# Kernel optimization log

Measured on AMD Instinct MI355X. Metric: run time of the kernel, lower is better.

## Reference

```python
import jax, jax.numpy as jnp
import numpy as np

V, O, E, D = 256, 128, 1024, 128
EPS = 1e-5


def setup_inputs() -> dict:
    key = jax.random.key(0)
    ks = jax.random.split(key, 8)
    inp = {}
    inp["obj_vecs"] = jax.random.normal(ks[0], (V, O, D), jnp.float32)
    inp["edges"] = jax.random.randint(ks[1], (V, E, 3), 0, O, dtype=jnp.int64)

    def lin(k, out_d, in_d):  # kaiming-ish init
        return jax.random.normal(k, (out_d, in_d), jnp.float32) * np.float32(np.sqrt(2.0 / in_d))

    i = 2
    for u in range(2):
        inp[f"u{u}_g1"] = jnp.ones((2 * D,), jnp.float32)
        inp[f"u{u}_b1"] = jnp.zeros((2 * D,), jnp.float32)
        inp[f"u{u}_W1"] = lin(ks[i], D, 2 * D); i += 1
        inp[f"u{u}_lb1"] = jnp.zeros((D,), jnp.float32)
        inp[f"u{u}_g2"] = jnp.ones((D,), jnp.float32)
        inp[f"u{u}_b2"] = jnp.zeros((D,), jnp.float32)
        inp[f"u{u}_W2"] = lin(ks[i], D, D); i += 1
        inp[f"u{u}_lb2"] = jnp.zeros((D,), jnp.float32)
    return inp


def _bn_relu(x, g, b):
    # training-mode BatchNorm1d (biased var) -> ReLU, pre-activation
    m = jnp.mean(x, axis=0)
    v = jnp.mean(jnp.square(x - m), axis=0)
    return jax.nn.relu((x - m) * jax.lax.rsqrt(v + EPS) * g + b)


def _gconv(x, s_flat, o_flat, p):
    g1, b1, W1, lb1, g2, b2, W2, lb2 = p
    xf = x.reshape(V * O, -1)
    # gather src/dst node features per edge -> (V*E, 2D)
    node = jnp.concatenate([xf[s_flat], xf[o_flat]], axis=-1)
    edge = _bn_relu(node, g1, b1) @ W1.T + lb1  # (V*E, Dedge)
    # scatter_add pooling onto source nodes, then average by in-count
    pooled = jax.ops.segment_sum(edge, s_flat, num_segments=V * O)
    cnt = jax.ops.segment_sum(jnp.ones((V * E,), edge.dtype), s_flat, num_segments=V * O)
    pooled = pooled / jnp.clip(cnt, 1.0)[:, None]
    out = _bn_relu(pooled, g2, b2) @ W2.T + lb2
    return out.reshape(V, O, -1)


def reference(obj_vecs, edges,
              u0_g1, u0_b1, u0_W1, u0_lb1, u0_g2, u0_b2, u0_W2, u0_lb2,
              u1_g1, u1_b1, u1_W1, u1_lb1, u1_g2, u1_b2, u1_W2, u1_lb2):
    off = (jnp.arange(V, dtype=edges.dtype) * O)[:, None]
    s_flat = (off + edges[:, :, 0]).reshape(-1)
    o_flat = (off + edges[:, :, 2]).reshape(-1)
    x = _gconv(obj_vecs, s_flat, o_flat,
               (u0_g1, u0_b1, u0_W1, u0_lb1, u0_g2, u0_b2, u0_W2, u0_lb2))
    x = _gconv(x, s_flat, o_flat,
               (u1_g1, u1_b1, u1_W1, u1_lb1, u1_g2, u1_b2, u1_W2, u1_lb2))
    return x + obj_vecs  # residual (input_dim == output_dim)
```

## Files before the change

kernel.cpp:

```cpp
#include <hip/hip_runtime.h>

namespace {
constexpr int kV = 256, kO = 128, kE = 1024, kD = 128;
constexpr int kN = kV * kO;
constexpr int kVE = kV * kE;
constexpr float kEps = 1e-5f;
}

typedef __attribute__((ext_vector_type(8))) short bf16x8;
typedef __attribute__((ext_vector_type(8))) unsigned short u16x8;
typedef __attribute__((ext_vector_type(4))) float f32x4;

__device__ __forceinline__ unsigned short f2bf(float x) {
  unsigned u = __float_as_uint(x);
  return (unsigned short)((u + 0x7FFFu + ((u >> 16) & 1u)) >> 16);
}
__device__ __forceinline__ float bf2f(unsigned short h) {
  return __uint_as_float((unsigned)h << 16);
}

__global__ __launch_bounds__(256) void k_adj(
    const unsigned int* __restrict__ ew, const float* __restrict__ X,
    int* __restrict__ cnt_s, int* __restrict__ cnt_o,
    unsigned short* __restrict__ Au16, float* __restrict__ p1) {
  __shared__ int cnt[kO * kO];
  __shared__ int degS[kO], degO[kO];
  __shared__ int anyodd;
  int v = blockIdx.x, t = threadIdx.x;
  if (t == 0) anyodd = 0;
  for (int i = t; i < kO * kO; i += 256) cnt[i] = 0;
  __syncthreads();
  int base = v * 3072, loc = 0;
  for (int i = t; i < 3072; i += 256) {
    int g = base + i;
    if ((g & 1) && ew[g] != 0u) loc = 1;
  }
  if (loc) atomicOr(&anyodd, 1);
  __syncthreads();
  bool is64 = (anyodd == 0);
  for (int e = t; e < kE; e += 256) {
    long long eb = (long long)(v * kE + e) * 3;
    unsigned s, o;
    if (is64) { s = ew[2 * eb]; o = ew[2 * (eb + 2)]; }
    else      { s = ew[eb];     o = ew[eb + 2]; }
    s &= 127u; o &= 127u;
    atomicAdd(&cnt[s * kO + o], 1);
  }
  __syncthreads();
  unsigned int* A32 = (unsigned int*)(Au16 + (size_t)v * 16384);
  for (int i2 = t; i2 < 8192; i2 += 256) {
    int i = 2 * i2;
    int row = i >> 7, k = i & 127, kg = k >> 3;
    int j = row * 128 + ((kg ^ (row & 7)) << 3) + (k & 7);
    unsigned lo = (unsigned)cnt[i], hi = (unsigned)cnt[i + 1];
    A32[j >> 1] = lo | (hi << 16);
  }
  if (t < kO) {
    int s = 0;
    for (int c = 0; c < kO; ++c) s += cnt[t * kO + ((c + t) & 127)];
    degS[t] = s;
    cnt_s[v * kO + t] = s;
  } else {
    int tc = t - kO;
    int s = 0;
    for (int r = 0; r < kO; ++r) s += cnt[((r + tc) & 127) * kO + tc];
    degO[tc] = s;
    cnt_o[v * kO + tc] = s;
  }
  __syncthreads();
  int dq = (t & 31) * 4, rg = t >> 5;
  float acc[4][4];
#pragma unroll
  for (int a = 0; a < 4; ++a)
#pragma unroll
    for (int j = 0; j < 4; ++j) acc[a][j] = 0.f;
  for (int k = 0; k < 16; ++k) {
    int row = rg + k * 8;
    float4 xv = *(const float4*)(X + ((size_t)v * kO + row) * kD + dq);
    float wsv = (float)degS[row], wov = (float)degO[row];
    float xs[4] = {xv.x, xv.y, xv.z, xv.w};
#pragma unroll
    for (int j = 0; j < 4; ++j) {
      acc[0][j] += wsv * xs[j];
      acc[1][j] += wsv * xs[j] * xs[j];
      acc[2][j] += wov * xs[j];
      acc[3][j] += wov * xs[j] * xs[j];
    }
  }
  float* red = (float*)cnt;
  for (int st = 0; st < 4; ++st) {
    __syncthreads();
#pragma unroll
    for (int j = 0; j < 4; ++j) red[rg * 128 + dq + j] = acc[st][j];
    __syncthreads();
    if (t < 128) {
      float s = 0.f;
#pragma unroll
      for (int g = 0; g < 8; ++g) s += red[g * 128 + t];
      p1[((size_t)v * 4 + st) * 128 + t] = s;
    }
  }
}

__global__ __launch_bounds__(256) void k_wsplit(
    const float* __restrict__ w1u0, const float* __restrict__ w2u0,
    const float* __restrict__ w1u1, const float* __restrict__ w2u1,
    unsigned short* __restrict__ img0,
    unsigned short* __restrict__ w2h0, unsigned short* __restrict__ w2l0,
    unsigned short* __restrict__ img1,
    unsigned short* __restrict__ w2h1, unsigned short* __restrict__ w2l1) {
  const float* w1s[2] = {w1u0, w1u1};
  const float* w2s[2] = {w2u0, w2u1};
  unsigned short* img[2] = {img0, img1};
  unsigned short* w2h[2] = {w2h0, w2h1};
  unsigned short* w2l[2] = {w2l0, w2l1};
  int i0 = blockIdx.x * 256 + threadIdx.x, stride = gridDim.x * 256;
#pragma unroll
  for (int u = 0; u < 2; ++u) {
    for (int i = i0; i < kD * 2 * kD; i += stride) {
      int j = i >> 8, k = i & 255;
      int m = k >> 7, kk = k & 127;
      int pos = j * 128 + (kk ^ ((j & 7) << 3));
      float x = w1s[u][i];
      unsigned short hb = f2bf(x);
      img[u][(m * 2 + 0) * 16384 + pos] = hb;
      img[u][(m * 2 + 1) * 16384 + pos] = f2bf(x - bf2f(hb));
    }
    for (int i = i0; i < kD * kD; i += stride) {
      float x = w2s[u][i];
      unsigned short hb = f2bf(x);
      w2h[u][i] = hb;
      w2l[u][i] = f2bf(x - bf2f(hb));
    }
  }
}

__global__ __launch_bounds__(256) void k_fin1(
    const float* __restrict__ p1, const float* __restrict__ g1,
    const float* __restrict__ b1, float* __restrict__ coef, int nslots) {
  __shared__ double sS[256], sQ[256];
  int c = blockIdx.x, t = threadIdx.x;
  int half = c >> 7, d = c & 127;
  double S = 0.0, Q = 0.0;
  for (int b = t; b < nslots; b += 256) {
    S += (double)p1[((size_t)b * 4 + half * 2 + 0) * 128 + d];
    Q += (double)p1[((size_t)b * 4 + half * 2 + 1) * 128 + d];
  }
  sS[t] = S; sQ[t] = Q;
  __syncthreads();
  for (int s = 128; s > 0; s >>= 1) {
    if (t < s) { sS[t] += sS[t + s]; sQ[t] += sQ[t + s]; }
    __syncthreads();
  }
  if (t == 0) {
    double m = sS[0] / (double)kVE;
    double var = sQ[0] / (double)kVE - m * m;
    float a = g1[c] / sqrtf((float)var + kEps);
    float beta = b1[c] - (float)m * a;
    coef[half * 256 + d] = a;
    coef[half * 256 + 128 + d] = beta;
  }
}

__global__ __launch_bounds__(512, 2) void k_fused1(
    const float* __restrict__ X, const unsigned short* __restrict__ w1img,
    const float* __restrict__ coef, const unsigned short* __restrict__ Au16,
    const int* __restrict__ cnt_s, const float* __restrict__ lb1,
    float* __restrict__ pooled, float* __restrict__ p2) {
  __shared__ __align__(16) unsigned short Wl[4][16384];
  int t = threadIdx.x, v = blockIdx.x;
  int lane = t & 63, wid = t >> 6;
  int wr = wid * 16, lrow = lane & 15, lkc = lane >> 4;
  int arow = wr + lrow;
#pragma unroll
  for (int a = 0; a < 4; ++a)
#pragma unroll
    for (int i = 0; i < 4; ++i)
      __builtin_amdgcn_global_load_lds(
          (const unsigned int*)((const char*)(w1img + a * 16384) +
                                wid * 4096 + i * 1024 + lane * 16),
          (unsigned int*)((char*)Wl[a] + wid * 4096 + i * 1024), 16, 0, 0);
  u16x8 au[4];
#pragma unroll
  for (int ks = 0; ks < 4; ++ks) {
    int kg = ks * 4 + lkc;
    au[ks] = *(const u16x8*)(Au16 + (size_t)v * 16384 + arow * 128 +
                             ((kg ^ (arow & 7)) << 3));
  }
  bf16x8 hsH[4], hsL[4], hoH[4], hoL[4];
#pragma unroll
  for (int ks = 0; ks < 4; ++ks) {
    int kb = ks * 32 + lkc * 8;
    float4 x0 = *(const float4*)(X + ((size_t)v * kO + arow) * kD + kb);
    float4 x1 = *(const float4*)(X + ((size_t)v * kO + arow) * kD + kb + 4);
    float4 aS0 = *(const float4*)(coef + kb),       aS1 = *(const float4*)(coef + kb + 4);
    float4 bS0 = *(const float4*)(coef + 128 + kb), bS1 = *(const float4*)(coef + 128 + kb + 4);
    float4 aO0 = *(const float4*)(coef + 256 + kb), aO1 = *(const float4*)(coef + 256 + kb + 4);
    float4 bO0 = *(const float4*)(coef + 384 + kb), bO1 = *(const float4*)(coef + 384 + kb + 4);
    float xs[8] = {x0.x, x0.y, x0.z, x0.w, x1.x, x1.y, x1.z, x1.w};
    float as[8] = {aS0.x, aS0.y, aS0.z, aS0.w, aS1.x, aS1.y, aS1.z, aS1.w};
    float bs[8] = {bS0.x, bS0.y, bS0.z, bS0.w, bS1.x, bS1.y, bS1.z, bS1.w};
    float ao[8] = {aO0.x, aO0.y, aO0.z, aO0.w, aO1.x, aO1.y, aO1.z, aO1.w};
    float bo[8] = {bO0.x, bO0.y, bO0.z, bO0.w, bO1.x, bO1.y, bO1.z, bO1.w};
#pragma unroll
    for (int e = 0; e < 8; ++e) {
      float hs = fmaxf(as[e] * xs[e] + bs[e], 0.f);
      float ho = fmaxf(ao[e] * xs[e] + bo[e], 0.f);
      unsigned short h1 = f2bf(hs);
      hsH[ks][e] = (short)h1;
      hsL[ks][e] = (short)f2bf(hs - bf2f(h1));
      unsigned short h2 = f2bf(ho);
      hoH[ks][e] = (short)h2;
      hoL[ks][e] = (short)f2bf(ho - bf2f(h2));
    }
  }
  __syncthreads();
  f32x4 accS[8], accO[8];
#pragma unroll
  for (int j = 0; j < 8; ++j) {
    accS[j] = (f32x4){0.f, 0.f, 0.f, 0.f};
    accO[j] = (f32x4){0.f, 0.f, 0.f, 0.f};
  }
#pragma unroll
  for (int ks = 0; ks < 4; ++ks) {
    int kb = ks * 32 + lkc * 8;
#pragma unroll
    for (int jg = 0; jg < 8; ++jg) {
      int j = jg * 16 + lrow;
      int idx = j * 128 + (kb ^ ((j & 7) << 3));
      bf16x8 bsh = *(const bf16x8*)(&Wl[0][idx]);
      bf16x8 bsl = *(const bf16x8*)(&Wl[1][idx]);
      bf16x8 boh = *(const bf16x8*)(&Wl[2][idx]);
      bf16x8 bol = *(const bf16x8*)(&Wl[3][idx]);
      accS[jg] = __builtin_amdgcn_mfma_f32_16x16x32_bf16(hsH[ks], bsh, accS[jg], 0, 0, 0);
      accS[jg] = __builtin_amdgcn_mfma_f32_16x16x32_bf16(hsH[ks], bsl, accS[jg], 0, 0, 0);
      accS[jg] = __builtin_amdgcn_mfma_f32_16x16x32_bf16(hsL[ks], bsh, accS[jg], 0, 0, 0);
      accO[jg] = __builtin_amdgcn_mfma_f32_16x16x32_bf16(hoH[ks], boh, accO[jg], 0, 0, 0);
      accO[jg] = __builtin_amdgcn_mfma_f32_16x16x32_bf16(hoH[ks], bol, accO[jg], 0, 0, 0);
      accO[jg] = __builtin_amdgcn_mfma_f32_16x16x32_bf16(hoL[ks], boh, accO[jg], 0, 0, 0);
    }
  }
  __syncthreads();
#pragma unroll
  for (int jg = 0; jg < 8; ++jg) {
    int d = jg * 16 + lrow;
#pragma unroll
    for (int q = 0; q < 4; ++q) {
      int o = wr + lkc * 4 + q;
      int addr = d * 128 + (o ^ ((d & 7) << 3));
      float vv = accO[jg][q];
      unsigned short h = f2bf(vv);
      Wl[0][addr] = h;
      Wl[1][addr] = f2bf(vv - bf2f(h));
    }
  }
  __syncthreads();
  f32x4 accP[8];
#pragma unroll
  for (int j = 0; j < 8; ++j) accP[j] = (f32x4){0.f, 0.f, 0.f, 0.f};
#pragma unroll
  for (int ks = 0; ks < 4; ++ks) {
    int kb = ks * 32 + lkc * 8;
    bf16x8 pah, pal;
#pragma unroll
    for (int e = 0; e < 8; ++e) {
      float c = (float)au[ks][e];
      unsigned short hb = f2bf(c);
      pah[e] = (short)hb;
      pal[e] = (short)f2bf(c - bf2f(hb));
    }
#pragma unroll
    for (int jg = 0; jg < 8; ++jg) {
      int d = jg * 16 + lrow;
      int qi = d * 128 + (kb ^ ((d & 7) << 3));
      bf16x8 qh = *(const bf16x8*)(&Wl[0][qi]), ql = *(const bf16x8*)(&Wl[1][qi]);
      accP[jg] = __builtin_amdgcn_mfma_f32_16x16x32_bf16(pah, qh, accP[jg], 0, 0, 0);
      accP[jg] = __builtin_amdgcn_mfma_f32_16x16x32_bf16(pah, ql, accP[jg], 0, 0, 0);
      accP[jg] = __builtin_amdgcn_mfma_f32_16x16x32_bf16(pal, qh, accP[jg], 0, 0, 0);
    }
  }
  float lb[8];
#pragma unroll
  for (int jg = 0; jg < 8; ++jg) lb[jg] = lb1[jg * 16 + lrow];
  float sm[8], sq[8];
#pragma unroll
  for (int jg = 0; jg < 8; ++jg) { sm[jg] = 0.f; sq[jg] = 0.f; }
#pragma unroll
  for (int q = 0; q < 4; ++q) {
    int row = wr + lkc * 4 + q;
    size_t n = (size_t)v * kO + row;
    int cnt = cnt_s[n];
    float inv = (cnt > 0) ? 1.f / (float)cnt : 0.f;
#pragma unroll
    for (int jg = 0; jg < 8; ++jg) {
      int col = jg * 16 + lrow;
      float pv = 0.f;
      if (cnt > 0) pv = accS[jg][q] + lb[jg] + accP[jg][q] * inv;
      pooled[n * kD + col] = pv;
      sm[jg] += pv; sq[jg] += pv * pv;
    }
  }
  float* red = (float*)Wl[2];
  int slot = wid * 4 + lkc;
#pragma unroll
  for (int jg = 0; jg < 8; ++jg) red[slot * 128 + jg * 16 + lrow] = sm[jg];
  __syncthreads();
  if (t < 128) {
    float s = 0.f;
#pragma unroll
    for (int g = 0; g < 32; ++g) s += red[g * 128 + t];
    p2[((size_t)v * 2 + 0) * 128 + t] = s;
  }
  __syncthreads();
#pragma unroll
  for (int jg = 0; jg < 8; ++jg) red[slot * 128 + jg * 16 + lrow] = sq[jg];
  __syncthreads();
  if (t < 128) {
    float s = 0.f;
#pragma unroll
    for (int g = 0; g < 32; ++g) s += red[g * 128 + t];
    p2[((size_t)v * 2 + 1) * 128 + t] = s;
  }
}

__global__ __launch_bounds__(256) void k_fin2(
    const float* __restrict__ p2, const float* __restrict__ g2,
    const float* __restrict__ b2, float* __restrict__ coef2) {
  __shared__ double sS[256], sQ[256];
  int d = blockIdx.x, t = threadIdx.x;
  double S = (double)p2[((size_t)t * 2 + 0) * 128 + d];
  double Q = (double)p2[((size_t)t * 2 + 1) * 128 + d];
  sS[t] = S; sQ[t] = Q;
  __syncthreads();
  for (int s = 128; s > 0; s >>= 1) {
    if (t < s) { sS[t] += sS[t + s]; sQ[t] += sQ[t + s]; }
    __syncthreads();
  }
  if (t == 0) {
    double m = sS[0] / (double)kN, var = sQ[0] / (double)kN - m * m;
    float a = g2[d] / sqrtf((float)var + kEps);
    float beta = b2[d] - (float)m * a;
    coef2[d] = a; coef2[128 + d] = beta;
  }
}

template <int STATS>
__global__ __launch_bounds__(256, 2) void k_gemm(
    const float* __restrict__ X,
    const unsigned short* __restrict__ Whi, const unsigned short* __restrict__ Wlo,
    const float* __restrict__ coefA, const float* __restrict__ coefB,
    float* __restrict__ Y, const float* __restrict__ bias, const float* __restrict__ resid,
    const int* __restrict__ cnt_s, const int* __restrict__ cnt_o,
    float* __restrict__ p1out) {
  __shared__ __align__(16) unsigned short AhL[8192], AlL[8192];
  int t = threadIdx.x, rb = blockIdx.x;
  int dq = (t & 31) * 4, rg = t >> 5;
  float4 av = *(const float4*)(coefA + dq);
  float4 bv = *(const float4*)(coefB + dq);
  for (int k = 0; k < 8; ++k) {
    int r = rg + k * 8;
    float4 xv = *(const float4*)(X + ((size_t)rb * 64 + r) * kD + dq);
    float h[4] = {fmaxf(av.x * xv.x + bv.x, 0.f), fmaxf(av.y * xv.y + bv.y, 0.f),
                  fmaxf(av.z * xv.z + bv.z, 0.f), fmaxf(av.w * xv.w + bv.w, 0.f)};
    ushort4 hi, lo;
    hi.x = f2bf(h[0]); lo.x = f2bf(h[0] - bf2f(hi.x));
    hi.y = f2bf(h[1]); lo.y = f2bf(h[1] - bf2f(hi.y));
    hi.z = f2bf(h[2]); lo.z = f2bf(h[2] - bf2f(hi.z));
    hi.w = f2bf(h[3]); lo.w = f2bf(h[3] - bf2f(hi.w));
    int idx = r * 128 + (dq ^ ((r & 7) << 3));
    *(ushort4*)(AhL + idx) = hi;
    *(ushort4*)(AlL + idx) = lo;
  }
  __syncthreads();
  int lane = t & 63, wid = t >> 6;
  int rh = wid & 1, ch = wid >> 1;
  int wr = rh * 32, lrow = lane & 15, lkc = lane >> 4;
  f32x4 acc[2][4];
#pragma unroll
  for (int i = 0; i < 2; ++i)
#pragma unroll
    for (int j = 0; j < 4; ++j) acc[i][j] = (f32x4){0.f, 0.f, 0.f, 0.f};
  for (int ks = 0; ks < 4; ++ks) {
    int kb = ks * 32 + lkc * 8;
    bf16x8 ah[2], al[2];
#pragma unroll
    for (int ri = 0; ri < 2; ++ri) {
      int ar = wr + ri * 16 + lrow;
      int ai = ar * 128 + (kb ^ ((ar & 7) << 3));
      ah[ri] = *(const bf16x8*)(AhL + ai);
      al[ri] = *(const bf16x8*)(AlL + ai);
    }
    bf16x8 bh[4], bl[4];
#pragma unroll
    for (int jg = 0; jg < 4; ++jg) {
      size_t wo = (size_t)(ch * 64 + jg * 16 + lrow) * 128 + kb;
      bh[jg] = *(const bf16x8*)(Whi + wo);
      bl[jg] = *(const bf16x8*)(Wlo + wo);
    }
#pragma unroll
    for (int jg = 0; jg < 4; ++jg)
#pragma unroll
      for (int ri = 0; ri < 2; ++ri) {
        acc[ri][jg] = __builtin_amdgcn_mfma_f32_16x16x32_bf16(ah[ri], bh[jg], acc[ri][jg], 0, 0, 0);
        acc[ri][jg] = __builtin_amdgcn_mfma_f32_16x16x32_bf16(ah[ri], bl[jg], acc[ri][jg], 0, 0, 0);
        acc[ri][jg] = __builtin_amdgcn_mfma_f32_16x16x32_bf16(al[ri], bh[jg], acc[ri][jg], 0, 0, 0);
      }
  }
  float s0[4], s1[4], s2[4], s3[4];
  if (STATS) {
#pragma unroll
    for (int jg = 0; jg < 4; ++jg) { s0[jg] = 0.f; s1[jg] = 0.f; s2[jg] = 0.f; s3[jg] = 0.f; }
  }
#pragma unroll
  for (int ri = 0; ri < 2; ++ri) {
    float wsr[4], wor[4];
    if (STATS) {
#pragma unroll
      for (int q = 0; q < 4; ++q) {
        int n = rb * 64 + wr + ri * 16 + lkc * 4 + q;
        wsr[q] = (float)cnt_s[n]; wor[q] = (float)cnt_o[n];
      }
    }
#pragma unroll
    for (int jg = 0; jg < 4; ++jg) {
      int col = ch * 64 + jg * 16 + lrow;
      float bcol = bias ? bias[col] : 0.f;
#pragma unroll
      for (int q = 0; q < 4; ++q) {
        int row = wr + ri * 16 + lkc * 4 + q;
        size_t n = (size_t)rb * 64 + row;
        float vv = acc[ri][jg][q] + bcol;
        if (resid) vv += resid[n * kD + col];
        Y[n * kD + col] = vv;
        if (STATS) {
          s0[jg] += wsr[q] * vv; s1[jg] += wsr[q] * vv * vv;
          s2[jg] += wor[q] * vv; s3[jg] += wor[q] * vv * vv;
        }
      }
    }
  }
  if (STATS) {
    __syncthreads();
    float* red = (float*)AhL;
    int slot = rh * 4 + lkc;
#pragma unroll
    for (int jg = 0; jg < 4; ++jg) {
      int col = ch * 64 + jg * 16 + lrow;
      red[0 * 1024 + slot * 128 + col] = s0[jg];
      red[1 * 1024 + slot * 128 + col] = s1[jg];
      red[2 * 1024 + slot * 128 + col] = s2[jg];
      red[3 * 1024 + slot * 128 + col] = s3[jg];
    }
    __syncthreads();
    if (t < 128) {
#pragma unroll
      for (int st = 0; st < 4; ++st) {
        float s = 0.f;
#pragma unroll
        for (int g = 0; g < 8; ++g) s += red[st * 1024 + g * 128 + t];
        p1out[((size_t)rb * 4 + st) * 128 + t] = s;
      }
    }
  }
}

extern "C" void kernel_launch(void* const* d_in, const int* in_sizes, int n_in,
                              void* d_out, int out_size, void* d_ws, size_t ws_size,
                              hipStream_t stream) {
  (void)in_sizes; (void)n_in; (void)out_size; (void)ws_size;
  const float* obj = (const float*)d_in[0];
  const unsigned int* ew = (const unsigned int*)d_in[1];
  const float* prm[2][8];
  for (int u = 0; u < 2; ++u)
    for (int p = 0; p < 8; ++p) prm[u][p] = (const float*)d_in[2 + u * 8 + p];

  char* ws = (char*)d_ws;
  size_t off = 0;
  auto carve = [&](size_t bytes) -> char* {
    char* p = ws + off;
    off = (off + bytes + 255) & ~(size_t)255;
    return p;
  };
  int* cnt_s = (int*)carve((size_t)kN * 4);
  int* cnt_o = (int*)carve((size_t)kN * 4);
  unsigned short* Au16 = (unsigned short*)carve((size_t)kV * 16384 * 2);
  float* p1 = (float*)carve((size_t)512 * 4 * 128 * 4);
  float* p2 = (float*)carve((size_t)kV * 2 * 128 * 4);
  float* coef1 = (float*)carve(512 * 4);
  float* coef2 = (float*)carve(256 * 4);
  unsigned short *w1img[2], *w2hi[2], *w2lo[2];
  for (int u = 0; u < 2; ++u) {
    w1img[u] = (unsigned short*)carve((size_t)4 * 16384 * 2);
    w2hi[u] = (unsigned short*)carve((size_t)kD * kD * 2);
    w2lo[u] = (unsigned short*)carve((size_t)kD * kD * 2);
  }
  float* pooled = (float*)carve((size_t)kN * kD * 4);
  float* x2 = (float*)carve((size_t)kN * kD * 4);

  k_adj<<<kV, 256, 0, stream>>>(ew, obj, cnt_s, cnt_o, Au16, p1);
  k_wsplit<<<128, 256, 0, stream>>>(prm[0][2], prm[0][6], prm[1][2], prm[1][6],
                                    w1img[0], w2hi[0], w2lo[0],
                                    w1img[1], w2hi[1], w2lo[1]);

  float* outp = (float*)d_out;
  k_fin1<<<256, 256, 0, stream>>>(p1, prm[0][0], prm[0][1], coef1, 256);
  k_fused1<<<kV, 512, 0, stream>>>(obj, w1img[0], coef1, Au16,
                                   cnt_s, prm[0][3], pooled, p2);
  k_fin2<<<128, 256, 0, stream>>>(p2, prm[0][4], prm[0][5], coef2);
  k_gemm<1><<<512, 256, 0, stream>>>(pooled, w2hi[0], w2lo[0], coef2, coef2 + 128,
                                     x2, prm[0][7], nullptr, cnt_s, cnt_o, p1);
  k_fin1<<<256, 256, 0, stream>>>(p1, prm[1][0], prm[1][1], coef1, 512);
  k_fused1<<<kV, 512, 0, stream>>>(x2, w1img[1], coef1, Au16,
                                   cnt_s, prm[1][3], pooled, p2);
  k_fin2<<<128, 256, 0, stream>>>(p2, prm[1][4], prm[1][5], coef2);
  k_gemm<0><<<512, 256, 0, stream>>>(pooled, w2hi[1], w2lo[1], coef2, coef2 + 128,
                                     outp, prm[1][7], obj, nullptr, nullptr, nullptr);
}
```

Baseline: 113.2 us.

## Stage W2 in LDS via async loads and keep activations in registers in k_gemm

The second-layer GEMM now uses 128-row tiles with 512 threads. The swizzled bf16 hi/lo W2 image is loaded into LDS with global_load_lds, where the old code read W2 fragments from global memory in every wave. Each wave builds its BN+ReLU split activations directly in registers, so the A-tile LDS staging and one barrier are gone. The cost is 64KB of LDS per block, which may limit occupancy, and a larger 32-slot stats reduction.

```diff
diff --git a/kernel.cpp b/kernel.cpp
--- a/kernel.cpp
+++ b/kernel.cpp
@@ -105,15 +105,12 @@
 __global__ __launch_bounds__(256) void k_wsplit(
     const float* __restrict__ w1u0, const float* __restrict__ w2u0,
     const float* __restrict__ w1u1, const float* __restrict__ w2u1,
-    unsigned short* __restrict__ img0,
-    unsigned short* __restrict__ w2h0, unsigned short* __restrict__ w2l0,
-    unsigned short* __restrict__ img1,
-    unsigned short* __restrict__ w2h1, unsigned short* __restrict__ w2l1) {
+    unsigned short* __restrict__ img0, unsigned short* __restrict__ w2img0,
+    unsigned short* __restrict__ img1, unsigned short* __restrict__ w2img1) {
   const float* w1s[2] = {w1u0, w1u1};
   const float* w2s[2] = {w2u0, w2u1};
   unsigned short* img[2] = {img0, img1};
-  unsigned short* w2h[2] = {w2h0, w2h1};
-  unsigned short* w2l[2] = {w2l0, w2l1};
+  unsigned short* w2i[2] = {w2img0, w2img1};
   int i0 = blockIdx.x * 256 + threadIdx.x, stride = gridDim.x * 256;
 #pragma unroll
   for (int u = 0; u < 2; ++u) {
@@ -127,10 +124,12 @@
       img[u][(m * 2 + 1) * 16384 + pos] = f2bf(x - bf2f(hb));
     }
     for (int i = i0; i < kD * kD; i += stride) {
+      int j = i >> 7, kk = i & 127;
+      int pos = j * 128 + (kk ^ ((j & 7) << 3));
       float x = w2s[u][i];
       unsigned short hb = f2bf(x);
-      w2h[u][i] = hb;
-      w2l[u][i] = f2bf(x - bf2f(hb));
+      w2i[u][pos] = hb;
+      w2i[u][16384 + pos] = f2bf(x - bf2f(hb));
     }
   }
 }
@@ -345,111 +344,103 @@
 }
 
 template <int STATS>
-__global__ __launch_bounds__(256, 2) void k_gemm(
-    const float* __restrict__ X,
-    const unsigned short* __restrict__ Whi, const unsigned short* __restrict__ Wlo,
+__global__ __launch_bounds__(512, 2) void k_gemm(
+    const float* __restrict__ X, const unsigned short* __restrict__ w2img,
     const float* __restrict__ coefA, const float* __restrict__ coefB,
     float* __restrict__ Y, const float* __restrict__ bias, const float* __restrict__ resid,
     const int* __restrict__ cnt_s, const int* __restrict__ cnt_o,
     float* __restrict__ p1out) {
-  __shared__ __align__(16) unsigned short AhL[8192], AlL[8192];
+  __shared__ __align__(16) unsigned short Wl[2][16384];
   int t = threadIdx.x, rb = blockIdx.x;
-  int dq = (t & 31) * 4, rg = t >> 5;
-  float4 av = *(const float4*)(coefA + dq);
-  float4 bv = *(const float4*)(coefB + dq);
-  for (int k = 0; k < 8; ++k) {
-    int r = rg + k * 8;
-    float4 xv = *(const float4*)(X + ((size_t)rb * 64 + r) * kD + dq);
-    float h[4] = {fmaxf(av.x * xv.x + bv.x, 0.f), fmaxf(av.y * xv.y + bv.y, 0.f),
-                  fmaxf(av.z * xv.z + bv.z, 0.f), fmaxf(av.w * xv.w + bv.w, 0.f)};
-    ushort4 hi, lo;
-    hi.x = f2bf(h[0]); lo.x = f2bf(h[0] - bf2f(hi.x));
-    hi.y = f2bf(h[1]); lo.y = f2bf(h[1] - bf2f(hi.y));
-    hi.z = f2bf(h[2]); lo.z = f2bf(h[2] - bf2f(hi.z));
-    hi.w = f2bf(h[3]); lo.w = f2bf(h[3] - bf2f(hi.w));
-    int idx = r * 128 + (dq ^ ((r & 7) << 3));
-    *(ushort4*)(AhL + idx) = hi;
-    *(ushort4*)(AlL + idx) = lo;
-  }
-  __syncthreads();
   int lane = t & 63, wid = t >> 6;
-  int rh = wid & 1, ch = wid >> 1;
-  int wr = rh * 32, lrow = lane & 15, lkc = lane >> 4;
-  f32x4 acc[2][4];
-#pragma unroll
-  for (int i = 0; i < 2; ++i)
-#pragma unroll
-    for (int j = 0; j < 4; ++j) acc[i][j] = (f32x4){0.f, 0.f, 0.f, 0.f};
+  int wr = wid * 16, lrow = lane & 15, lkc = lane >> 4;
+  int arow = wr + lrow;
+#pragma unroll
+  for (int a = 0; a < 2; ++a)
+#pragma unroll
+    for (int i = 0; i < 4; ++i)
+      __builtin_amdgcn_global_load_lds(
+          (const unsigned int*)((const char*)(w2img + a * 16384) +
+                                wid * 4096 + i * 1024 + lane * 16),
+          (unsigned int*)((char*)Wl[a] + wid * 4096 + i * 1024), 16, 0, 0);
+  bf16x8 ahH[4], ahL[4];
+#pragma unroll
   for (int ks = 0; ks < 4; ++ks) {
     int kb = ks * 32 + lkc * 8;
-    bf16x8 ah[2], al[2];
-#pragma unroll
-    for (int ri = 0; ri < 2; ++ri) {
-      int ar = wr + ri * 16 + lrow;
-      int ai = ar * 128 + (kb ^ ((ar & 7) << 3));
-      ah[ri] = *(const bf16x8*)(AhL + ai);
-      al[ri] = *(const bf16x8*)(AlL + ai);
-    }
-    bf16x8 bh[4], bl[4];
-#pragma unroll
-    for (int jg = 0; jg < 4; ++jg) {
-      size_t wo = (size_t)(ch * 64 + jg * 16 + lrow) * 128 + kb;
-      bh[jg] = *(const bf16x8*)(Whi + wo);
-      bl[jg] = *(const bf16x8*)(Wlo + wo);
-    }
-#pragma unroll
-    for (int jg = 0; jg < 4; ++jg)
-#pragma unroll
-      for (int ri = 0; ri < 2; ++ri) {
-        acc[ri][jg] = __builtin_amdgcn_mfma_f32_16x16x32_bf16(ah[ri], bh[jg], acc[ri][jg], 0, 0, 0);
-        acc[ri][jg] = __builtin_amdgcn_mfma_f32_16x16x32_bf16(ah[ri], bl[jg], acc[ri][jg], 0, 0, 0);
-        acc[ri][jg] = __builtin_amdgcn_mfma_f32_16x16x32_bf16(al[ri], bh[jg], acc[ri][jg], 0, 0, 0);
-      }
-  }
-  float s0[4], s1[4], s2[4], s3[4];
+    float4 x0 = *(const float4*)(X + ((size_t)rb * kO + arow) * kD + kb);
+    float4 x1 = *(const float4*)(X + ((size_t)rb * kO + arow) * kD + kb + 4);
+    float4 a0 = *(const float4*)(coefA + kb), a1 = *(const float4*)(coefA + kb + 4);
+    float4 b0 = *(const float4*)(coefB + kb), b1 = *(const float4*)(coefB + kb + 4);
+    float xs[8] = {x0.x, x0.y, x0.z, x0.w, x1.x, x1.y, x1.z, x1.w};
+    float as[8] = {a0.x, a0.y, a0.z, a0.w, a1.x, a1.y, a1.z, a1.w};
+    float bs[8] = {b0.x, b0.y, b0.z, b0.w, b1.x, b1.y, b1.z, b1.w};
+#pragma unroll
+    for (int e = 0; e < 8; ++e) {
+      float h = fmaxf(as[e] * xs[e] + bs[e], 0.f);
+      unsigned short hb = f2bf(h);
+      ahH[ks][e] = (short)hb;
+      ahL[ks][e] = (short)f2bf(h - bf2f(hb));
+    }
+  }
+  __syncthreads();
+  f32x4 acc[8];
+#pragma unroll
+  for (int j = 0; j < 8; ++j) acc[j] = (f32x4){0.f, 0.f, 0.f, 0.f};
+#pragma unroll
+  for (int ks = 0; ks < 4; ++ks) {
+    int kb = ks * 32 + lkc * 8;
+#pragma unroll
+    for (int jg = 0; jg < 8; ++jg) {
+      int j = jg * 16 + lrow;
+      int idx = j * 128 + (kb ^ ((j & 7) << 3));
+      bf16x8 bh = *(const bf16x8*)(&Wl[0][idx]);
+      bf16x8 bl = *(const bf16x8*)(&Wl[1][idx]);
+      acc[jg] = __builtin_amdgcn_mfma_f32_16x16x32_bf16(ahH[ks], bh, acc[jg], 0, 0, 0);
+      acc[jg] = __builtin_amdgcn_mfma_f32_16x16x32_bf16(ahH[ks], bl, acc[jg], 0, 0, 0);
+      acc[jg] = __builtin_amdgcn_mfma_f32_16x16x32_bf16(ahL[ks], bh, acc[jg], 0, 0, 0);
+    }
+  }
+  float s0[8], s1[8], s2[8], s3[8];
   if (STATS) {
 #pragma unroll
-    for (int jg = 0; jg < 4; ++jg) { s0[jg] = 0.f; s1[jg] = 0.f; s2[jg] = 0.f; s3[jg] = 0.f; }
-  }
-#pragma unroll
-  for (int ri = 0; ri < 2; ++ri) {
-    float wsr[4], wor[4];
-    if (STATS) {
-#pragma unroll
-      for (int q = 0; q < 4; ++q) {
-        int n = rb * 64 + wr + ri * 16 + lkc * 4 + q;
-        wsr[q] = (float)cnt_s[n]; wor[q] = (float)cnt_o[n];
-      }
-    }
-#pragma unroll
-    for (int jg = 0; jg < 4; ++jg) {
-      int col = ch * 64 + jg * 16 + lrow;
-      float bcol = bias ? bias[col] : 0.f;
-#pragma unroll
-      for (int q = 0; q < 4; ++q) {
-        int row = wr + ri * 16 + lkc * 4 + q;
-        size_t n = (size_t)rb * 64 + row;
-        float vv = acc[ri][jg][q] + bcol;
-        if (resid) vv += resid[n * kD + col];
-        Y[n * kD + col] = vv;
-        if (STATS) {
-          s0[jg] += wsr[q] * vv; s1[jg] += wsr[q] * vv * vv;
-          s2[jg] += wor[q] * vv; s3[jg] += wor[q] * vv * vv;
-        }
+    for (int jg = 0; jg < 8; ++jg) { s0[jg] = 0.f; s1[jg] = 0.f; s2[jg] = 0.f; s3[jg] = 0.f; }
+  }
+  float wsr[4], wor[4];
+  if (STATS) {
+#pragma unroll
+    for (int q = 0; q < 4; ++q) {
+      int n = rb * kO + wr + lkc * 4 + q;
+      wsr[q] = (float)cnt_s[n]; wor[q] = (float)cnt_o[n];
+    }
+  }
+#pragma unroll
+  for (int jg = 0; jg < 8; ++jg) {
+    int col = jg * 16 + lrow;
+    float bcol = bias ? bias[col] : 0.f;
+#pragma unroll
+    for (int q = 0; q < 4; ++q) {
+      int row = wr + lkc * 4 + q;
+      size_t n = (size_t)rb * kO + row;
+      float vv = acc[jg][q] + bcol;
+      if (resid) vv += resid[n * kD + col];
+      Y[n * kD + col] = vv;
+      if (STATS) {
+        s0[jg] += wsr[q] * vv; s1[jg] += wsr[q] * vv * vv;
+        s2[jg] += wor[q] * vv; s3[jg] += wor[q] * vv * vv;
       }
     }
   }
   if (STATS) {
     __syncthreads();
-    float* red = (float*)AhL;
-    int slot = rh * 4 + lkc;
-#pragma unroll
-    for (int jg = 0; jg < 4; ++jg) {
-      int col = ch * 64 + jg * 16 + lrow;
-      red[0 * 1024 + slot * 128 + col] = s0[jg];
-      red[1 * 1024 + slot * 128 + col] = s1[jg];
-      red[2 * 1024 + slot * 128 + col] = s2[jg];
-      red[3 * 1024 + slot * 128 + col] = s3[jg];
+    float* red = (float*)Wl;
+    int slot = wid * 4 + lkc;
+#pragma unroll
+    for (int jg = 0; jg < 8; ++jg) {
+      int col = jg * 16 + lrow;
+      red[0 * 4096 + slot * 128 + col] = s0[jg];
+      red[1 * 4096 + slot * 128 + col] = s1[jg];
+      red[2 * 4096 + slot * 128 + col] = s2[jg];
+      red[3 * 4096 + slot * 128 + col] = s3[jg];
     }
     __syncthreads();
     if (t < 128) {
@@ -457,7 +448,7 @@
       for (int st = 0; st < 4; ++st) {
         float s = 0.f;
 #pragma unroll
-        for (int g = 0; g < 8; ++g) s += red[st * 1024 + g * 128 + t];
+        for (int g = 0; g < 32; ++g) s += red[st * 4096 + g * 128 + t];
         p1out[((size_t)rb * 4 + st) * 128 + t] = s;
       }
     }
@@ -484,35 +475,33 @@
   int* cnt_s = (int*)carve((size_t)kN * 4);
   int* cnt_o = (int*)carve((size_t)kN * 4);
   unsigned short* Au16 = (unsigned short*)carve((size_t)kV * 16384 * 2);
-  float* p1 = (float*)carve((size_t)512 * 4 * 128 * 4);
+  float* p1 = (float*)carve((size_t)256 * 4 * 128 * 4);
   float* p2 = (float*)carve((size_t)kV * 2 * 128 * 4);
   float* coef1 = (float*)carve(512 * 4);
   float* coef2 = (float*)carve(256 * 4);
-  unsigned short *w1img[2], *w2hi[2], *w2lo[2];
+  unsigned short *w1img[2], *w2img[2];
   for (int u = 0; u < 2; ++u) {
     w1img[u] = (unsigned short*)carve((size_t)4 * 16384 * 2);
-    w2hi[u] = (unsigned short*)carve((size_t)kD * kD * 2);
-    w2lo[u] = (unsigned short*)carve((size_t)kD * kD * 2);
+    w2img[u] = (unsigned short*)carve((size_t)2 * 16384 * 2);
   }
   float* pooled = (float*)carve((size_t)kN * kD * 4);
   float* x2 = (float*)carve((size_t)kN * kD * 4);
 
   k_adj<<<kV, 256, 0, stream>>>(ew, obj, cnt_s, cnt_o, Au16, p1);
   k_wsplit<<<128, 256, 0, stream>>>(prm[0][2], prm[0][6], prm[1][2], prm[1][6],
-                                    w1img[0], w2hi[0], w2lo[0],
-                                    w1img[1], w2hi[1], w2lo[1]);
+                                    w1img[0], w2img[0], w1img[1], w2img[1]);
 
   float* outp = (float*)d_out;
   k_fin1<<<256, 256, 0, stream>>>(p1, prm[0][0], prm[0][1], coef1, 256);
   k_fused1<<<kV, 512, 0, stream>>>(obj, w1img[0], coef1, Au16,
                                    cnt_s, prm[0][3], pooled, p2);
   k_fin2<<<128, 256, 0, stream>>>(p2, prm[0][4], prm[0][5], coef2);
-  k_gemm<1><<<512, 256, 0, stream>>>(pooled, w2hi[0], w2lo[0], coef2, coef2 + 128,
-                                     x2, prm[0][7], nullptr, cnt_s, cnt_o, p1);
-  k_fin1<<<256, 256, 0, stream>>>(p1, prm[1][0], prm[1][1], coef1, 512);
+  k_gemm<1><<<kV, 512, 0, stream>>>(pooled, w2img[0], coef2, coef2 + 128,
+                                    x2, prm[0][7], nullptr, cnt_s, cnt_o, p1);
+  k_fin1<<<256, 256, 0, stream>>>(p1, prm[1][0], prm[1][1], coef1, 256);
   k_fused1<<<kV, 512, 0, stream>>>(x2, w1img[1], coef1, Au16,
                                    cnt_s, prm[1][3], pooled, p2);
   k_fin2<<<128, 256, 0, stream>>>(p2, prm[1][4], prm[1][5], coef2);
-  k_gemm<0><<<512, 256, 0, stream>>>(pooled, w2hi[1], w2lo[1], coef2, coef2 + 128,
-                                     outp, prm[1][7], obj, nullptr, nullptr, nullptr);
-}
+  k_gemm<0><<<kV, 512, 0, stream>>>(pooled, w2img[1], coef2, coef2 + 128,
+                                    outp, prm[1][7], obj, nullptr, nullptr, nullptr);
+}
```

New measurement: 104.9 us. -7.3%, faster.
